# Kernel tuning notes

Hardware: AMD Instinct MI355X
Metric: run time of the kernel (lower is better)

## Reference

```python
import jax, jax.numpy as jnp
import numpy as np

M = 50000   # eval points
N = 1024    # gaussians
EPS = 1e-6


def setup_inputs() -> dict:
    key = jax.random.key(0)
    k1, k2, k3 = jax.random.split(key, 3)
    points = jax.random.uniform(k1, (M, 3), dtype=jnp.float32)          # normalized coords in [0,1)
    positions = jax.random.uniform(k2, (N, 3), dtype=jnp.float32)       # torch.rand init
    log_scales = jnp.full((N, 3), -3.0, dtype=jnp.float32)              # torch.full(..., -3.0)
    intensities = jax.random.uniform(k3, (N,), dtype=jnp.float32) * 0.5  # torch.rand * 0.5
    return {"points": points, "positions": positions,
            "log_scales": log_scales, "intensities": intensities}


def reference(points, positions, log_scales, intensities):
    # Faithful translation of FastGaussianModel._eval_gaussians
    scales = jnp.exp(log_scales)                      # [N,3]
    inv_var = 1.0 / (scales ** 2 + EPS)               # [N,3]
    diff = points[:, None, :] - positions[None, :, :] # [M,N,3]
    quad = jnp.einsum('mnd,nd->mn', diff * diff, inv_var)  # [M,N]
    gauss = jnp.exp(-0.5 * quad)                      # [M,N]
    values = gauss @ intensities                      # [M]
    return values
```

## Files before the change

### kernel.cpp

```cpp
#include <hip/hip_runtime.h>


typedef float v2f __attribute__((ext_vector_type(2)));

constexpr int BLOCK = 256;
constexpr int PTS_PER_BLOCK = 64;

__global__ void fgm_prep(const float* __restrict__ positions,
                         const float* __restrict__ log_scales,
                         const float* __restrict__ intensities,
                         float* __restrict__ coef, int N, int NpairsPad) {
    int i = blockIdx.x * blockDim.x + threadIdx.x;
    if (i >= NpairsPad) return;
    float v[2][8];
    for (int h = 0; h < 2; ++h) {
        int n = 2 * i + h;
        float a0=0.f,a1=0.f,a2=0.f,b0=0.f,b1=0.f,b2=0.f,c=0.f,w=0.f;
        if (n < N) {
            const float K = -0.7213475204444817f;
            float q0 = positions[3*n+0], q1 = positions[3*n+1], q2 = positions[3*n+2];
            float iv0 = 1.0f / (__expf(2.0f*log_scales[3*n+0]) + 1e-6f);
            float iv1 = 1.0f / (__expf(2.0f*log_scales[3*n+1]) + 1e-6f);
            float iv2 = 1.0f / (__expf(2.0f*log_scales[3*n+2]) + 1e-6f);
            a0 = K * (-2.f*iv0*q0);  b0 = K * iv0;
            a1 = K * (-2.f*iv1*q1);  b1 = K * iv1;
            a2 = K * (-2.f*iv2*q2);  b2 = K * iv2;
            c  = K * (iv0*q0*q0 + iv1*q1*q1 + iv2*q2*q2);
            w  = intensities[n];
        }
        v[h][0]=a0; v[h][1]=a1; v[h][2]=a2; v[h][3]=b0;
        v[h][4]=b1; v[h][5]=b2; v[h][6]=c;  v[h][7]=w;
    }
    float4* out = (float4*)(coef + (size_t)i * 16);
    out[0] = make_float4(v[0][0], v[1][0], v[0][1], v[1][1]);
    out[1] = make_float4(v[0][2], v[1][2], v[0][3], v[1][3]);
    out[2] = make_float4(v[0][4], v[1][4], v[0][5], v[1][5]);
    out[3] = make_float4(v[0][6], v[1][6], v[0][7], v[1][7]);
}

__global__ __launch_bounds__(BLOCK, 3) void fgm_main(const float* __restrict__ points,
                                                     const float* __restrict__ coef,
                                                     float* __restrict__ out,
                                                     int M, int pairsPerWave,
                                                     int NpairsPad) {
    __shared__ float red[4][PTS_PER_BLOCK];

    int lane = threadIdx.x & 63;
    int wave = __builtin_amdgcn_readfirstlane(threadIdx.x >> 6);

    int m = blockIdx.x * PTS_PER_BLOCK + lane;
    float px = 0.f, py = 0.f, pz = 0.f;
    if (m < M) {
        px = points[3*m+0];
        py = points[3*m+1];
        pz = points[3*m+2];
    }
    v2f vpx  = {px, px},       vpy  = {py, py},       vpz  = {pz, pz};
    v2f vpx2 = {px*px, px*px}, vpy2 = {py*py, py*py}, vpz2 = {pz*pz, pz*pz};

    int pairBase = wave * pairsPerWave;
    int pairEnd  = pairBase + pairsPerWave;
    if (pairEnd > NpairsPad) pairEnd = NpairsPad;

    const v2f* cp = (const v2f*)coef;
    v2f acc = {0.f, 0.f};
    #pragma unroll 4
    for (int i = pairBase; i < pairEnd; ++i) {
        v2f A0 = cp[8*i+0], A1 = cp[8*i+1], A2 = cp[8*i+2], B0 = cp[8*i+3];
        v2f B1 = cp[8*i+4], B2 = cp[8*i+5], C  = cp[8*i+6], W  = cp[8*i+7];
        v2f t = __builtin_elementwise_fma(A0, vpx,  C);
        t = __builtin_elementwise_fma(A1, vpy,  t);
        t = __builtin_elementwise_fma(A2, vpz,  t);
        t = __builtin_elementwise_fma(B0, vpx2, t);
        t = __builtin_elementwise_fma(B1, vpy2, t);
        t = __builtin_elementwise_fma(B2, vpz2, t);
        v2f g;
        g.x = __builtin_amdgcn_exp2f(t.x);
        g.y = __builtin_amdgcn_exp2f(t.y);
        acc = __builtin_elementwise_fma(g, W, acc);
    }

    red[wave][lane] = acc.x + acc.y;
    __syncthreads();
    if (wave == 0 && m < M) {
        out[m] = (red[0][lane] + red[1][lane]) + (red[2][lane] + red[3][lane]);
    }
}

extern "C" void kernel_launch(void* const* d_in, const int* in_sizes, int n_in,
                              void* d_out, int out_size, void* d_ws, size_t ws_size,
                              hipStream_t stream) {
    const float* points      = (const float*)d_in[0];
    const float* positions   = (const float*)d_in[1];
    const float* log_scales  = (const float*)d_in[2];
    const float* intensities = (const float*)d_in[3];
    int M = in_sizes[0] / 3;
    int N = in_sizes[3];

    int Npairs       = (N + 1) / 2;
    int pairsPerWave = (Npairs + 3) / 4;
    int NpairsPad    = pairsPerWave * 4;

    float* coef = (float*)d_ws;

    fgm_prep<<<(NpairsPad + 255) / 256, 256, 0, stream>>>(positions, log_scales,
                                                          intensities, coef,
                                                          N, NpairsPad);

    int blocks = (M + PTS_PER_BLOCK - 1) / PTS_PER_BLOCK;
    fgm_main<<<blocks, BLOCK, 0, stream>>>(points, coef, (float*)d_out,
                                           M, pairsPerWave, NpairsPad);
}
```

Baseline: 77.52 us.

## Register-tile 8 points per lane and split gaussians across a 2D grid with atomics

Each lane now evaluates 8 points, so every coefficient load is reused across 8 points instead of one. Gaussians are split into 32 slices spread over a second grid dimension, which keeps enough blocks in flight now that each block covers more points. Partial sums are combined with atomicAdd into an output zeroed by a memset. The costs are an extra memset launch, atomic traffic, higher register pressure, and results that can vary with atomic ordering.

```diff
diff --git a/kernel.cpp b/kernel.cpp
--- a/kernel.cpp
+++ b/kernel.cpp
@@ -3,8 +3,12 @@
 
 typedef float v2f __attribute__((ext_vector_type(2)));
 
-constexpr int BLOCK = 256;
-constexpr int PTS_PER_BLOCK = 64;
+constexpr int BLOCK           = 256;
+constexpr int WAVES_PER_BLOCK = 4;
+constexpr int PTS_PER_LANE    = 8;
+constexpr int TILE_PTS        = 64 * PTS_PER_LANE;
+constexpr int SLICE_GROUPS    = 8;
+constexpr int TOTAL_SLICES    = SLICE_GROUPS * WAVES_PER_BLOCK;
 
 __global__ void fgm_prep(const float* __restrict__ positions,
                          const float* __restrict__ log_scales,
@@ -38,52 +42,62 @@
     out[3] = make_float4(v[0][6], v[1][6], v[0][7], v[1][7]);
 }
 
-__global__ __launch_bounds__(BLOCK, 3) void fgm_main(const float* __restrict__ points,
-                                                     const float* __restrict__ coef,
-                                                     float* __restrict__ out,
-                                                     int M, int pairsPerWave,
-                                                     int NpairsPad) {
-    __shared__ float red[4][PTS_PER_BLOCK];
+__global__ __launch_bounds__(BLOCK) void fgm_main(const float* __restrict__ points,
+                                                  const float* __restrict__ coef,
+                                                  float* __restrict__ out,
+                                                  int M, int pairsPerSlice) {
+    __shared__ float red[WAVES_PER_BLOCK][TILE_PTS];
 
     int lane = threadIdx.x & 63;
     int wave = __builtin_amdgcn_readfirstlane(threadIdx.x >> 6);
+    int tileBase = blockIdx.x * TILE_PTS;
+    int slice = blockIdx.y * WAVES_PER_BLOCK + wave;
 
-    int m = blockIdx.x * PTS_PER_BLOCK + lane;
-    float px = 0.f, py = 0.f, pz = 0.f;
-    if (m < M) {
-        px = points[3*m+0];
-        py = points[3*m+1];
-        pz = points[3*m+2];
-    }
-    v2f vpx  = {px, px},       vpy  = {py, py},       vpz  = {pz, pz};
-    v2f vpx2 = {px*px, px*px}, vpy2 = {py*py, py*py}, vpz2 = {pz*pz, pz*pz};
-
-    int pairBase = wave * pairsPerWave;
-    int pairEnd  = pairBase + pairsPerWave;
-    if (pairEnd > NpairsPad) pairEnd = NpairsPad;
-
-    const v2f* cp = (const v2f*)coef;
-    v2f acc = {0.f, 0.f};
-    #pragma unroll 4
-    for (int i = pairBase; i < pairEnd; ++i) {
-        v2f A0 = cp[8*i+0], A1 = cp[8*i+1], A2 = cp[8*i+2], B0 = cp[8*i+3];
-        v2f B1 = cp[8*i+4], B2 = cp[8*i+5], C  = cp[8*i+6], W  = cp[8*i+7];
-        v2f t = __builtin_elementwise_fma(A0, vpx,  C);
-        t = __builtin_elementwise_fma(A1, vpy,  t);
-        t = __builtin_elementwise_fma(A2, vpz,  t);
-        t = __builtin_elementwise_fma(B0, vpx2, t);
-        t = __builtin_elementwise_fma(B1, vpy2, t);
-        t = __builtin_elementwise_fma(B2, vpz2, t);
-        v2f g;
-        g.x = __builtin_amdgcn_exp2f(t.x);
-        g.y = __builtin_amdgcn_exp2f(t.y);
-        acc = __builtin_elementwise_fma(g, W, acc);
+    float px[PTS_PER_LANE], py[PTS_PER_LANE], pz[PTS_PER_LANE];
+    float qx[PTS_PER_LANE], qy[PTS_PER_LANE], qz[PTS_PER_LANE];
+    v2f acc[PTS_PER_LANE];
+    #pragma unroll
+    for (int j = 0; j < PTS_PER_LANE; ++j) {
+        int m = tileBase + lane + 64 * j;
+        float x = 0.f, y = 0.f, z = 0.f;
+        if (m < M) { x = points[3*m+0]; y = points[3*m+1]; z = points[3*m+2]; }
+        px[j] = x;   py[j] = y;   pz[j] = z;
+        qx[j] = x*x; qy[j] = y*y; qz[j] = z*z;
+        acc[j] = (v2f){0.f, 0.f};
     }
 
-    red[wave][lane] = acc.x + acc.y;
+    const v2f* cp = (const v2f*)coef + (size_t)slice * pairsPerSlice * 8;
+    #pragma unroll 2
+    for (int i = 0; i < pairsPerSlice; ++i) {
+        v2f A0 = cp[0], A1 = cp[1], A2 = cp[2], B0 = cp[3];
+        v2f B1 = cp[4], B2 = cp[5], C  = cp[6], W  = cp[7];
+        cp += 8;
+        #pragma unroll
+        for (int j = 0; j < PTS_PER_LANE; ++j) {
+            v2f t = __builtin_elementwise_fma(A0, (v2f){px[j], px[j]}, C);
+            t = __builtin_elementwise_fma(A1, (v2f){py[j], py[j]}, t);
+            t = __builtin_elementwise_fma(A2, (v2f){pz[j], pz[j]}, t);
+            t = __builtin_elementwise_fma(B0, (v2f){qx[j], qx[j]}, t);
+            t = __builtin_elementwise_fma(B1, (v2f){qy[j], qy[j]}, t);
+            t = __builtin_elementwise_fma(B2, (v2f){qz[j], qz[j]}, t);
+            v2f g;
+            g.x = __builtin_amdgcn_exp2f(t.x);
+            g.y = __builtin_amdgcn_exp2f(t.y);
+            acc[j] = __builtin_elementwise_fma(g, W, acc[j]);
+        }
+    }
+
+    #pragma unroll
+    for (int j = 0; j < PTS_PER_LANE; ++j)
+        red[wave][lane + 64 * j] = acc[j].x + acc[j].y;
     __syncthreads();
-    if (wave == 0 && m < M) {
-        out[m] = (red[0][lane] + red[1][lane]) + (red[2][lane] + red[3][lane]);
+
+    for (int p = threadIdx.x; p < TILE_PTS; p += BLOCK) {
+        int m = tileBase + p;
+        if (m < M) {
+            float s = (red[0][p] + red[1][p]) + (red[2][p] + red[3][p]);
+            atomicAdd(&out[m], s);
+        }
     }
 }
 
@@ -97,17 +111,20 @@
     int M = in_sizes[0] / 3;
     int N = in_sizes[3];
 
-    int Npairs       = (N + 1) / 2;
-    int pairsPerWave = (Npairs + 3) / 4;
-    int NpairsPad    = pairsPerWave * 4;
+    int Npairs        = (N + 1) / 2;
+    int pairsPerSlice = (Npairs + TOTAL_SLICES - 1) / TOTAL_SLICES;
+    int NpairsPad     = pairsPerSlice * TOTAL_SLICES;
 
     float* coef = (float*)d_ws;
+
+    hipMemsetAsync(d_out, 0, (size_t)out_size * sizeof(float), stream);
 
     fgm_prep<<<(NpairsPad + 255) / 256, 256, 0, stream>>>(positions, log_scales,
                                                           intensities, coef,
                                                           N, NpairsPad);
 
-    int blocks = (M + PTS_PER_BLOCK - 1) / PTS_PER_BLOCK;
-    fgm_main<<<blocks, BLOCK, 0, stream>>>(points, coef, (float*)d_out,
-                                           M, pairsPerWave, NpairsPad);
+    int tiles = (M + TILE_PTS - 1) / TILE_PTS;
+    dim3 grid(tiles, SLICE_GROUPS);
+    fgm_main<<<grid, BLOCK, 0, stream>>>(points, coef, (float*)d_out,
+                                         M, pairsPerSlice);
 }
```

After: 78.10 us. About the same (+0.7%).
